# Performance work log

Hardware: AMD Instinct MI355X
Metric: run time of the kernel (lower is better)

The kernel has to match this reference:

```python
import jax, jax.numpy as jnp
import numpy as np

B, LQ, LKV = 2, 4096, 1024
QUERY_DIM, CROSS_DIM = 512, 768
HEADS, DIM_HEAD = 8, 64
INNER = HEADS * DIM_HEAD
SCALE = DIM_HEAD ** -0.5


def setup_inputs() -> dict:
    key = jax.random.key(0)
    ks = jax.random.split(key, 7)
    s = 0.02
    return {
        "hidden_states": jax.random.normal(ks[0], (B, LQ, QUERY_DIM), jnp.float32),
        "encoder_hidden_states": jax.random.normal(ks[1], (B, LKV, CROSS_DIM), jnp.float32),
        "Wq": jax.random.normal(ks[2], (QUERY_DIM, INNER), jnp.float32) * s,
        "Wk": jax.random.normal(ks[3], (CROSS_DIM, INNER), jnp.float32) * s,
        "Wv": jax.random.normal(ks[4], (CROSS_DIM, INNER), jnp.float32) * s,
        "Wo": jax.random.normal(ks[5], (INNER, QUERY_DIM), jnp.float32) * s,
        "bo": jnp.zeros((QUERY_DIM,), jnp.float32),
    }


def reference(hidden_states, encoder_hidden_states, Wq, Wk, Wv, Wo, bo):
    # Projections
    q = hidden_states @ Wq                 # [B, Lq, inner]
    k = encoder_hidden_states @ Wk         # [B, Lkv, inner]
    v = encoder_hidden_states @ Wv         # [B, Lkv, inner]
    # Split heads: [B, H, L, Dh]
    q = q.reshape(B, LQ, HEADS, DIM_HEAD).transpose(0, 2, 1, 3)
    k = k.reshape(B, LKV, HEADS, DIM_HEAD).transpose(0, 2, 1, 3)
    v = v.reshape(B, LKV, HEADS, DIM_HEAD).transpose(0, 2, 1, 3)
    # Scores [B, H, Lq, Lkv], softmax over Lkv
    scores = jnp.einsum("bhqd,bhkd->bhqk", q, k) * SCALE
    attn = jax.nn.softmax(scores, axis=-1)
    out = jnp.einsum("bhqk,bhkd->bhqd", attn, v)  # [B, H, Lq, Dh]
    out = out.transpose(0, 2, 1, 3).reshape(B, LQ, INNER)
    return out @ Wo + bo                   # [B, Lq, query_dim]
```

## Files before the change

kernel.cpp:

```cpp
#include <hip/hip_runtime.h>
#include <hip/hip_bf16.h>
#include <math.h>

#define BB 2
#define LQ 4096
#define LKV 1024
#define QDIM 512
#define CDIM 768
#define HEADS 8
#define DHEAD 64
#define INNER 512
#define SCALE 0.125f

#define C1 0.18033688011112042f
#define C2 5.7707801635558535f

typedef __bf16 bf16x4 __attribute__((ext_vector_type(4)));
typedef __bf16 bf16x8 __attribute__((ext_vector_type(8)));
typedef float f32x4 __attribute__((ext_vector_type(4)));

__global__ __launch_bounds__(256)
void prep_weights(const float* __restrict__ Wq, const float* __restrict__ Wk,
                  const float* __restrict__ Wv, const float* __restrict__ Wo,
                  __bf16* __restrict__ Wq_t, __bf16* __restrict__ Wkv_t,
                  __bf16* __restrict__ Wo_t) {
    __shared__ float tile[32][33];
    int id = blockIdx.x;
    const float* W; __bf16* Out; int K;
    if (id < 256)       { W = Wq; Out = Wq_t; K = 512; }
    else if (id < 640)  { id -= 256;  W = Wk; Out = Wkv_t; K = 768; }
    else if (id < 1024) { id -= 640;  W = Wv; Out = Wkv_t + (size_t)512 * 768; K = 768; }
    else                { id -= 1024; W = Wo; Out = Wo_t; K = 512; }
    const int NT = 512 / 32;
    int kt = id / NT, nt = id % NT;
    const int t = threadIdx.x;
    int r = t >> 3, c4 = (t & 7) * 4;
    float4 v = *(const float4*)&W[(size_t)(kt * 32 + r) * 512 + nt * 32 + c4];
    tile[r][c4 + 0] = v.x; tile[r][c4 + 1] = v.y; tile[r][c4 + 2] = v.z; tile[r][c4 + 3] = v.w;
    __syncthreads();
    bf16x4 o = { (__bf16)tile[c4 + 0][r], (__bf16)tile[c4 + 1][r],
                 (__bf16)tile[c4 + 2][r], (__bf16)tile[c4 + 3][r] };
    *(bf16x4*)&Out[(size_t)(nt * 32 + r) * K + kt * 32 + c4] = o;
}

template<int BM, int BN, int BK, bool AF32, bool F32OUT, bool VTEP>
__global__ __launch_bounds__(256)
void gemm_t(const void* __restrict__ Av, const __bf16* __restrict__ Bt,
            __bf16* __restrict__ Cb, float* __restrict__ Cf, const float* __restrict__ bias,
            __bf16* __restrict__ VT, int M, int N, int K, int CN) {
    static_assert(BK == 64, "swizzle assumes 128-byte rows");
    constexpr int WM = BM / 2, WN = BN / 2, FM = WM / 16, FN = WN / 16;
    constexpr int KK = BK / 32;
    constexpr int AQ4 = BM * BK / 1024;
    constexpr int AC8 = BM * BK / 2048;
    constexpr int BC8 = BN * BK / 2048;
    __shared__ __align__(16) __bf16 As[2][BM * BK];
    __shared__ __align__(16) __bf16 Bs[2][BN * BK];
    const int t = threadIdx.x;
    const int lane = t & 63;
    const int w = t >> 6;
    const int wm = w >> 1, wn = w & 1;
    const int bm = blockIdx.x * BM, bn = blockIdx.y * BN;
    const float* Af = (const float*)Av;
    const __bf16* Ab = (const __bf16*)Av;
    f32x4 acc[FM][FN] = {};
    const int rr = lane & 15, kb8 = (lane >> 4) * 8;
    const int rsw = (rr & 7) << 4;
    const int NK = K / BK;

    float4 rA[AQ4];
    bf16x8 rAb[AC8];
    bf16x8 rB[BC8];

    auto loadA = [&](int kt) {
        if (AF32) {
            #pragma unroll
            for (int j = 0; j < AQ4; j++) {
                int q = t + 256 * j;
                rA[j] = *(const float4*)&Af[(size_t)(bm + (q >> 4)) * K + kt * BK + (q & 15) * 4];
            }
        } else {
            #pragma unroll
            for (int j = 0; j < AC8; j++) {
                int c = t + 256 * j;
                rAb[j] = *(const bf16x8*)&Ab[(size_t)(bm + (c >> 3)) * K + kt * BK + (c & 7) * 8];
            }
        }
    };
    auto loadB = [&](int kt) {
        #pragma unroll
        for (int j = 0; j < BC8; j++) {
            int c = t + 256 * j;
            rB[j] = *(const bf16x8*)&Bt[(size_t)(bn + (c >> 3)) * K + kt * BK + (c & 7) * 8];
        }
    };
    auto writeBuf = [&](int buf) {
        if (AF32) {
            #pragma unroll
            for (int j = 0; j < AQ4; j++) {
                int q = t + 256 * j;
                bf16x4 o = { (__bf16)rA[j].x, (__bf16)rA[j].y, (__bf16)rA[j].z, (__bf16)rA[j].w };
                int row = q >> 4;
                *(bf16x4*)((char*)As[buf] + ((q * 8) ^ ((row & 7) << 4))) = o;
            }
        } else {
            #pragma unroll
            for (int j = 0; j < AC8; j++) {
                int c = t + 256 * j;
                int row = c >> 3;
                *(bf16x8*)((char*)As[buf] + ((c * 16) ^ ((row & 7) << 4))) = rAb[j];
            }
        }
        #pragma unroll
        for (int j = 0; j < BC8; j++) {
            int c = t + 256 * j;
            int row = c >> 3;
            *(bf16x8*)((char*)Bs[buf] + ((c * 16) ^ ((row & 7) << 4))) = rB[j];
        }
    };

    loadA(0); loadB(0);
    writeBuf(0);
    if (NK > 1) { loadA(1); loadB(1); }
    __syncthreads();

    for (int kt = 0; kt < NK; kt++) {
        const int cur = kt & 1;
        if (kt > 0) __syncthreads();
        if (kt + 1 < NK) writeBuf(cur ^ 1);
        if (kt + 2 < NK) { loadA(kt + 2); loadB(kt + 2); }
        #pragma unroll
        for (int kk = 0; kk < KK; kk++) {
            bf16x8 a[FM], b[FN];
            #pragma unroll
            for (int f = 0; f < FM; f++)
                a[f] = *(const bf16x8*)((const char*)As[cur] +
                    (((wm * WM + f * 16 + rr) * 128 + kk * 64 + kb8 * 2) ^ rsw));
            #pragma unroll
            for (int f = 0; f < FN; f++)
                b[f] = *(const bf16x8*)((const char*)Bs[cur] +
                    (((wn * WN + f * 16 + rr) * 128 + kk * 64 + kb8 * 2) ^ rsw));
            __builtin_amdgcn_s_setprio(1);
            #pragma unroll
            for (int fm = 0; fm < FM; fm++)
                #pragma unroll
                for (int fn = 0; fn < FN; fn++)
                    acc[fm][fn] = __builtin_amdgcn_mfma_f32_16x16x32_bf16(a[fm], b[fn], acc[fm][fn], 0, 0, 0);
            __builtin_amdgcn_s_setprio(0);
        }
    }

    const int colg = lane & 15;
    const int rowg = (lane >> 4) * 4;
    if (VTEP && bn >= 512) {
        __syncthreads();
        __bf16* T = &As[0][0];
        #pragma unroll
        for (int fm = 0; fm < FM; fm++)
            #pragma unroll
            for (int fn = 0; fn < FN; fn++) {
                int dcol = wn * WN + fn * 16 + colg;
                int kvr  = wm * WM + fm * 16 + rowg;
                bf16x4 pv = { (__bf16)acc[fm][fn][0], (__bf16)acc[fm][fn][1],
                              (__bf16)acc[fm][fn][2], (__bf16)acc[fm][fn][3] };
                *(bf16x4*)((char*)T + ((dcol * 128 + kvr * 2) ^ ((dcol & 7) << 4))) = pv;
            }
        __syncthreads();
        int d = t >> 2, ch = t & 3;
        int base = d * 128 + ch * 32;
        bf16x8 o0 = *(const bf16x8*)((const char*)T + ((base) ^ ((d & 7) << 4)));
        bf16x8 o1 = *(const bf16x8*)((const char*)T + ((base + 16) ^ ((d & 7) << 4)));
        int b = bm >> 10, kv0 = bm & 1023, h = (bn - 512) >> 6;
        size_t vrow = (size_t)((b * 8 + h) * 64 + d);
        *(bf16x8*)&VT[vrow * 1024 + kv0 + ch * 16] = o0;
        *(bf16x8*)&VT[vrow * 1024 + kv0 + ch * 16 + 8] = o1;
    } else {
        #pragma unroll
        for (int fm = 0; fm < FM; fm++)
            #pragma unroll
            for (int fn = 0; fn < FN; fn++)
                #pragma unroll
                for (int r = 0; r < 4; r++) {
                    int row = bm + wm * WM + fm * 16 + rowg + r;
                    int col = bn + wn * WN + fn * 16 + colg;
                    float v = acc[fm][fn][r];
                    if (F32OUT) Cf[(size_t)row * CN + col] = v + bias[col];
                    else        Cb[(size_t)row * CN + col] = (__bf16)v;
                }
    }
}

__global__ __launch_bounds__(512, 4)
void attn4(const __bf16* __restrict__ Q, const __bf16* __restrict__ Kb,
           const __bf16* __restrict__ VT, __bf16* __restrict__ O) {
    __shared__ __align__(16) __bf16 SQ[128 * 64];
    __shared__ __align__(16) __bf16 Ks[2][64 * 64];
    __shared__ __align__(16) __bf16 Vs[2][64 * 64];
    const int t = threadIdx.x;
    const int lane = t & 63;
    const int w = t >> 6;
    const int bh = blockIdx.y;
    const int b = bh >> 3, h = bh & 7;
    const int qbase = b * LQ + blockIdx.x * 128;
    const int kvbase = b * LKV;
    const int hq = h * 64;
    const int q16 = lane & 15;
    const int hh = lane >> 4;

    #pragma unroll
    for (int i = 0; i < 2; i++) {
        int c = t + 512 * i;
        int row = c >> 3;
        bf16x8 v = *(const bf16x8*)&Q[(size_t)(qbase + row) * INNER + hq + (c & 7) * 8];
        *(bf16x8*)((char*)SQ + ((row * 128 + (c & 7) * 16) ^ ((row & 7) << 4))) = v;
    }

    const int srow = t >> 3;
    const int soff = ((srow * 128 + (t & 7) * 16) ^ ((srow & 7) << 4));
    bf16x8 kr, vr;
    kr = *(const bf16x8*)&Kb[(size_t)(kvbase + srow) * 512 + hq + (t & 7) * 8];
    vr = *(const bf16x8*)&VT[((size_t)bh * 64 + srow) * 1024 + (t & 7) * 8];
    *(bf16x8*)((char*)Ks[0] + soff) = kr;
    *(bf16x8*)((char*)Vs[0] + soff) = vr;
    kr = *(const bf16x8*)&Kb[(size_t)(kvbase + 64 + srow) * 512 + hq + (t & 7) * 8];
    vr = *(const bf16x8*)&VT[((size_t)bh * 64 + srow) * 1024 + 64 + (t & 7) * 8];
    __syncthreads();

    const int qrow = w * 16 + q16;
    const int rsw = (q16 & 7) << 4;
    bf16x8 qf0 = *(const bf16x8*)((const char*)SQ + ((qrow * 128 + hh * 16) ^ rsw));
    bf16x8 qf1 = *(const bf16x8*)((const char*)SQ + ((qrow * 128 + 64 + hh * 16) ^ rsw));
    bf16x8 ones;
    #pragma unroll
    for (int j = 0; j < 8; j++) ones[j] = (__bf16)1.0f;

    f32x4 acc_o[4] = {};
    f32x4 acc_l = {};

    const int NT = LKV / 64;
    for (int kt = 0; kt < NT; kt++) {
        const int cur = kt & 1;
        if (kt > 0) __syncthreads();
        if (kt + 1 < NT) {
            const int nxt = cur ^ 1;
            *(bf16x8*)((char*)Ks[nxt] + soff) = kr;
            *(bf16x8*)((char*)Vs[nxt] + soff) = vr;
        }
        if (kt + 2 < NT) {
            kr = *(const bf16x8*)&Kb[(size_t)(kvbase + (kt + 2) * 64 + srow) * 512 + hq + (t & 7) * 8];
            vr = *(const bf16x8*)&VT[((size_t)bh * 64 + srow) * 1024 + (kt + 2) * 64 + (t & 7) * 8];
        }

        f32x4 s[4];
        __builtin_amdgcn_s_setprio(1);
        #pragma unroll
        for (int kvf = 0; kvf < 4; kvf++) {
            int krow = kvf * 16 + q16;
            bf16x8 k0 = *(const bf16x8*)((const char*)Ks[cur] + ((krow * 128 + hh * 16) ^ rsw));
            bf16x8 k1 = *(const bf16x8*)((const char*)Ks[cur] + ((krow * 128 + 64 + hh * 16) ^ rsw));
            f32x4 sa = {};
            sa = __builtin_amdgcn_mfma_f32_16x16x32_bf16(k0, qf0, sa, 0, 0, 0);
            sa = __builtin_amdgcn_mfma_f32_16x16x32_bf16(k1, qf1, sa, 0, 0, 0);
            s[kvf] = sa;
        }
        __builtin_amdgcn_s_setprio(0);

        #pragma unroll
        for (int kvf = 0; kvf < 4; kvf++) {
            bf16x4 pv;
            #pragma unroll
            for (int r = 0; r < 4; r++)
                pv[r] = (__bf16)exp2f(__builtin_fmaf(s[kvf][r], C1, -C2));
            *(bf16x4*)((char*)SQ + ((qrow * 128 + kvf * 32 + hh * 8) ^ rsw)) = pv;
        }
        bf16x8 pa0 = *(const bf16x8*)((const char*)SQ + ((qrow * 128 + hh * 16) ^ rsw));
        bf16x8 pa1 = *(const bf16x8*)((const char*)SQ + ((qrow * 128 + 64 + hh * 16) ^ rsw));

        __builtin_amdgcn_s_setprio(1);
        acc_l = __builtin_amdgcn_mfma_f32_16x16x32_bf16(pa0, ones, acc_l, 0, 0, 0);
        acc_l = __builtin_amdgcn_mfma_f32_16x16x32_bf16(pa1, ones, acc_l, 0, 0, 0);
        #pragma unroll
        for (int df = 0; df < 4; df++) {
            int vrow = df * 16 + q16;
            bf16x8 v0 = *(const bf16x8*)((const char*)Vs[cur] + ((vrow * 128 + hh * 16) ^ rsw));
            bf16x8 v1 = *(const bf16x8*)((const char*)Vs[cur] + ((vrow * 128 + 64 + hh * 16) ^ rsw));
            acc_o[df] = __builtin_amdgcn_mfma_f32_16x16x32_bf16(pa0, v0, acc_o[df], 0, 0, 0);
            acc_o[df] = __builtin_amdgcn_mfma_f32_16x16x32_bf16(pa1, v1, acc_o[df], 0, 0, 0);
        }
        __builtin_amdgcn_s_setprio(0);
    }

    #pragma unroll
    for (int df = 0; df < 4; df++)
        #pragma unroll
        for (int r = 0; r < 4; r++) {
            float v = acc_o[df][r] / acc_l[r];
            int row = w * 16 + hh * 4 + r;
            int col = df * 16 + q16;
            *(__bf16*)((char*)SQ + ((row * 128 + col * 2) ^ ((row & 7) << 4))) = (__bf16)v;
        }
    __syncthreads();
    #pragma unroll
    for (int i = 0; i < 2; i++) {
        int c = t + 512 * i;
        int row = c >> 3;
        bf16x8 v = *(const bf16x8*)((const char*)SQ + ((row * 128 + (c & 7) * 16) ^ ((row & 7) << 4)));
        *(bf16x8*)&O[(size_t)(qbase + row) * INNER + hq + (c & 7) * 8] = v;
    }
}

extern "C" void kernel_launch(void* const* d_in, const int* in_sizes, int n_in,
                              void* d_out, int out_size, void* d_ws, size_t ws_size,
                              hipStream_t stream) {
    const float* hs  = (const float*)d_in[0];
    const float* ehs = (const float*)d_in[1];
    const float* Wq  = (const float*)d_in[2];
    const float* Wk  = (const float*)d_in[3];
    const float* Wv  = (const float*)d_in[4];
    const float* Wo  = (const float*)d_in[5];
    const float* bo  = (const float*)d_in[6];
    float* out = (float*)d_out;

    char* ws = (char*)d_ws;
    size_t off = 0;
    auto alloc = [&](size_t nbytes) {
        char* p = ws + off;
        off += (nbytes + 255) & ~(size_t)255;
        return p;
    };
    __bf16* Wq_t  = (__bf16*)alloc((size_t)QDIM * INNER * 2);
    __bf16* Wkv_t = (__bf16*)alloc((size_t)CDIM * INNER * 2 * 2);
    __bf16* Wo_t  = (__bf16*)alloc((size_t)INNER * QDIM * 2);
    __bf16* Qb    = (__bf16*)alloc((size_t)BB * LQ * INNER * 2);
    __bf16* Kbb   = (__bf16*)alloc((size_t)BB * LKV * INNER * 2);
    __bf16* VTb   = (__bf16*)alloc((size_t)BB * HEADS * DHEAD * LKV * 2);
    __bf16* AOb   = (__bf16*)alloc((size_t)BB * LQ * INNER * 2);

    prep_weights<<<dim3(1280), dim3(256), 0, stream>>>(Wq, Wk, Wv, Wo, Wq_t, Wkv_t, Wo_t);

    gemm_t<64, 128, 64, true, false, false><<<dim3(BB * LQ / 64, INNER / 128), dim3(256), 0, stream>>>(
        hs, Wq_t, Qb, nullptr, nullptr, nullptr, BB * LQ, INNER, QDIM, INNER);
    gemm_t<64, 64, 64, true, false, true><<<dim3(BB * LKV / 64, 1024 / 64), dim3(256), 0, stream>>>(
        ehs, Wkv_t, Kbb, nullptr, nullptr, VTb, BB * LKV, 1024, CDIM, INNER);
    attn4<<<dim3(LQ / 128, BB * HEADS), dim3(512), 0, stream>>>(Qb, Kbb, VTb, AOb);
    gemm_t<64, 128, 64, false, true, false><<<dim3(BB * LQ / 64, QDIM / 128), dim3(256), 0, stream>>>(
        AOb, Wo_t, nullptr, out, bo, nullptr, BB * LQ, QDIM, INNER, QDIM);
}
```

Before: 74.27 us.

## Use direct global-to-LDS loads for bf16 GEMM operand tiles

Replaces the register-staged loading of bf16 A and B tiles with global_load_lds instructions that write straight into shared memory. The swizzle moves from the LDS write address to the global read column so the layout matches the existing conflict-free reads. The aim is to save VGPRs and the LDS store instructions and to overlap loads with MFMA. The barrier moves to the end of each k-iteration. Correctness relies on the compiler inserting waits for the async LDS loads before the barrier, and prefetch depth drops from two stages to one.

```diff
diff --git a/kernel.cpp b/kernel.cpp
--- a/kernel.cpp
+++ b/kernel.cpp
@@ -18,6 +18,11 @@
 typedef __bf16 bf16x4 __attribute__((ext_vector_type(4)));
 typedef __bf16 bf16x8 __attribute__((ext_vector_type(8)));
 typedef float f32x4 __attribute__((ext_vector_type(4)));
+
+__device__ inline void gload16(const void* g, void* l) {
+    __builtin_amdgcn_global_load_lds((const __attribute__((address_space(1))) unsigned int*)g,
+                                     (__attribute__((address_space(3))) unsigned int*)l, 16, 0, 0);
+}
 
 __global__ __launch_bounds__(256)
 void prep_weights(const float* __restrict__ Wq, const float* __restrict__ Wk,
@@ -69,66 +74,56 @@
     const int NK = K / BK;
 
     float4 rA[AQ4];
-    bf16x8 rAb[AC8];
-    bf16x8 rB[BC8];
 
     auto loadA = [&](int kt) {
-        if (AF32) {
-            #pragma unroll
-            for (int j = 0; j < AQ4; j++) {
-                int q = t + 256 * j;
-                rA[j] = *(const float4*)&Af[(size_t)(bm + (q >> 4)) * K + kt * BK + (q & 15) * 4];
-            }
-        } else {
-            #pragma unroll
-            for (int j = 0; j < AC8; j++) {
-                int c = t + 256 * j;
-                rAb[j] = *(const bf16x8*)&Ab[(size_t)(bm + (c >> 3)) * K + kt * BK + (c & 7) * 8];
-            }
-        }
-    };
-    auto loadB = [&](int kt) {
-        #pragma unroll
-        for (int j = 0; j < BC8; j++) {
+        #pragma unroll
+        for (int j = 0; j < AQ4; j++) {
+            int q = t + 256 * j;
+            rA[j] = *(const float4*)&Af[(size_t)(bm + (q >> 4)) * K + kt * BK + (q & 15) * 4];
+        }
+    };
+    auto writeA = [&](int buf) {
+        #pragma unroll
+        for (int j = 0; j < AQ4; j++) {
+            int q = t + 256 * j;
+            bf16x4 o = { (__bf16)rA[j].x, (__bf16)rA[j].y, (__bf16)rA[j].z, (__bf16)rA[j].w };
+            int row = q >> 4;
+            *(bf16x4*)((char*)As[buf] + ((q * 8) ^ ((row & 7) << 4))) = o;
+        }
+    };
+    auto issueA = [&](int kt, int buf) {
+        #pragma unroll
+        for (int j = 0; j < AC8; j++) {
             int c = t + 256 * j;
-            rB[j] = *(const bf16x8*)&Bt[(size_t)(bn + (c >> 3)) * K + kt * BK + (c & 7) * 8];
-        }
-    };
-    auto writeBuf = [&](int buf) {
-        if (AF32) {
-            #pragma unroll
-            for (int j = 0; j < AQ4; j++) {
-                int q = t + 256 * j;
-                bf16x4 o = { (__bf16)rA[j].x, (__bf16)rA[j].y, (__bf16)rA[j].z, (__bf16)rA[j].w };
-                int row = q >> 4;
-                *(bf16x4*)((char*)As[buf] + ((q * 8) ^ ((row & 7) << 4))) = o;
-            }
-        } else {
-            #pragma unroll
-            for (int j = 0; j < AC8; j++) {
-                int c = t + 256 * j;
-                int row = c >> 3;
-                *(bf16x8*)((char*)As[buf] + ((c * 16) ^ ((row & 7) << 4))) = rAb[j];
-            }
-        }
+            int row = c >> 3;
+            int kc = (c & 7) ^ (row & 7);
+            gload16(&Ab[(size_t)(bm + row) * K + kt * BK + kc * 8],
+                    (char*)As[buf] + (w * 64 + 256 * j) * 16);
+        }
+    };
+    auto issueB = [&](int kt, int buf) {
         #pragma unroll
         for (int j = 0; j < BC8; j++) {
             int c = t + 256 * j;
             int row = c >> 3;
-            *(bf16x8*)((char*)Bs[buf] + ((c * 16) ^ ((row & 7) << 4))) = rB[j];
-        }
-    };
-
-    loadA(0); loadB(0);
-    writeBuf(0);
-    if (NK > 1) { loadA(1); loadB(1); }
+            int kc = (c & 7) ^ (row & 7);
+            gload16(&Bt[(size_t)(bn + row) * K + kt * BK + kc * 8],
+                    (char*)Bs[buf] + (w * 64 + 256 * j) * 16);
+        }
+    };
+
+    if (AF32) { loadA(0); writeA(0); if (NK > 1) loadA(1); }
+    else issueA(0, 0);
+    issueB(0, 0);
     __syncthreads();
 
     for (int kt = 0; kt < NK; kt++) {
         const int cur = kt & 1;
-        if (kt > 0) __syncthreads();
-        if (kt + 1 < NK) writeBuf(cur ^ 1);
-        if (kt + 2 < NK) { loadA(kt + 2); loadB(kt + 2); }
+        if (kt + 1 < NK) {
+            issueB(kt + 1, cur ^ 1);
+            if (AF32) { writeA(cur ^ 1); if (kt + 2 < NK) loadA(kt + 2); }
+            else issueA(kt + 1, cur ^ 1);
+        }
         #pragma unroll
         for (int kk = 0; kk < KK; kk++) {
             bf16x8 a[FM], b[FN];
@@ -148,12 +143,12 @@
                     acc[fm][fn] = __builtin_amdgcn_mfma_f32_16x16x32_bf16(a[fm], b[fn], acc[fm][fn], 0, 0, 0);
             __builtin_amdgcn_s_setprio(0);
         }
+        __syncthreads();
     }
 
     const int colg = lane & 15;
     const int rowg = (lane >> 4) * 4;
     if (VTEP && bn >= 512) {
-        __syncthreads();
         __bf16* T = &As[0][0];
         #pragma unroll
         for (int fm = 0; fm < FM; fm++)
```

Measured after the change: 74.31 us. About the same (+0.1%).
